# Kernel tuning notes

Hardware: AMD Instinct MI355X
Metric: run time of the kernel (lower is better)

## Reference

```python
import jax, jax.numpy as jnp
import numpy as np

SEQ_LEN = 4096
EMBED_DIM = 1024
NUM_HEADS = 16  # head_dim = 64


def setup_inputs() -> dict:
    key = jax.random.key(0)
    k0, k1, k2 = jax.random.split(key, 3)
    std = 0.02
    x = jax.random.normal(k0, (SEQ_LEN, EMBED_DIM), dtype=jnp.float32)
    # torch Linear convention: weight [out_features, in_features], y = x @ W.T + b
    W_qkv = jax.random.normal(k1, (3 * EMBED_DIM, EMBED_DIM), dtype=jnp.float32) * std
    b_qkv = jnp.zeros((3 * EMBED_DIM,), dtype=jnp.float32)
    W_out = jax.random.normal(k2, (EMBED_DIM, EMBED_DIM), dtype=jnp.float32) * std
    b_out = jnp.zeros((EMBED_DIM,), dtype=jnp.float32)
    return {"input": x, "W_qkv": W_qkv, "b_qkv": b_qkv, "W_out": W_out, "b_out": b_out}


def reference(input, W_qkv, b_qkv, W_out, b_out):
    S, E = input.shape
    H = NUM_HEADS
    Dh = E // H
    # fused QKV projection: [S, 3E]
    projected = input @ W_qkv.T + b_qkv
    q, k, v = jnp.split(projected, 3, axis=1)          # each [S, E]
    q = q.reshape(S, H, Dh)
    k = k.reshape(S, H, Dh)
    v = v.reshape(S, H, Dh)
    # unscaled attention (the original applies no 1/sqrt(d) scaling)
    scores = jnp.einsum('shd,thd->hst', q, k)          # [H, S, S] -- full matrix in HBM
    probs = jax.nn.softmax(scores, axis=-1)
    out = jnp.einsum('hst,thd->shd', probs, v)         # [S, H, Dh]
    out = out.reshape(S, E)
    return out @ W_out.T + b_out
```

## Files before the change

kernel.cpp:

```cpp
#include <hip/hip_runtime.h>

typedef unsigned short u16;
typedef short    bf16x8 __attribute__((ext_vector_type(8)));
typedef u16      u16x8  __attribute__((ext_vector_type(8)));
typedef u16      u16x4  __attribute__((ext_vector_type(4)));
typedef float    f32x4  __attribute__((ext_vector_type(4)));
typedef unsigned u32x2  __attribute__((ext_vector_type(2)));

__device__ __forceinline__ u16 f2bf(float f) {
  unsigned x = __float_as_uint(f);
  unsigned r = x + 0x7fffu + ((x >> 16) & 1u);
  return (u16)(r >> 16);
}
__device__ __forceinline__ float bf2f(u16 u) {
  return __uint_as_float(((unsigned)u) << 16);
}
__device__ __forceinline__ float exp2v(float x) {
  float r;
  asm("v_exp_f32 %0, %1" : "=v"(r) : "v"(x));
  return r;
}

__global__ __launch_bounds__(256) void cast3(const float* __restrict__ x,
                                             const float* __restrict__ wq,
                                             const float* __restrict__ wo,
                                             u16* __restrict__ xb,
                                             u16* __restrict__ wqb,
                                             u16* __restrict__ wob) {
  int b = blockIdx.x;
  const float* s; u16* d; int i;
  if (b < 4096)      { s = x;  d = xb;  i = b * 256 + threadIdx.x; }
  else if (b < 7168) { s = wq; d = wqb; i = (b - 4096) * 256 + threadIdx.x; }
  else               { s = wo; d = wob; i = (b - 7168) * 256 + threadIdx.x; }
  f32x4 v = ((const f32x4*)s)[i];
  u16x4 o;
  o[0] = f2bf(v[0]); o[1] = f2bf(v[1]); o[2] = f2bf(v[2]); o[3] = f2bf(v[3]);
  ((u16x4*)d)[i] = o;
}

template<int N, int K, bool OUTF32, bool SCALEQ, bool VSPLIT>
__global__ __launch_bounds__(256) void gemm_bt(const u16* __restrict__ A,
                                               const u16* __restrict__ B,
                                               const float* __restrict__ bias,
                                               void* __restrict__ Cout,
                                               u16* __restrict__ vtout) {
  __shared__ __align__(16) u16 smem[16384];
  const int tid = threadIdx.x;
  const int flat = blockIdx.y * gridDim.x + blockIdx.x;
  const int q8 = (gridDim.x * gridDim.y) >> 3;
  const int sw = (flat & 7) * q8 + (flat >> 3);
  const int m0 = (sw / gridDim.x) * 128, n0 = (sw % gridDim.x) * 128;
  const int wave = tid >> 6, lane = tid & 63;
  const int c = lane & 15, g = lane >> 4;
  const int wm = (wave >> 1) * 64, wn = (wave & 1) * 64;
  f32x4 acc[4][4] = {};

  const int sr = wave * 16 + (lane >> 2);
  const int sc = (lane & 3) * 8;

  auto stage = [&](int buf, int k0) {
#pragma unroll
    for (int j = 0; j < 2; j++) {
      __builtin_amdgcn_global_load_lds(
        (const __attribute__((address_space(1))) void*)(A + (size_t)(m0 + j * 64 + sr) * K + k0 + sc),
        (__attribute__((address_space(3))) void*)&smem[buf * 4096 + (j * 64 + wave * 16) * 32], 16, 0, 0);
      __builtin_amdgcn_global_load_lds(
        (const __attribute__((address_space(1))) void*)(B + (size_t)(n0 + j * 64 + sr) * K + k0 + sc),
        (__attribute__((address_space(3))) void*)&smem[8192 + buf * 4096 + (j * 64 + wave * 16) * 32], 16, 0, 0);
    }
  };

  stage(0, 0);
  __syncthreads();

  const int nT = K / 32;
  for (int t = 0; t < nT; ++t) {
    const int buf = t & 1;
    if (t + 1 < nT) stage(buf ^ 1, (t + 1) * 32);
    bf16x8 af[4], bfr[4];
#pragma unroll
    for (int m = 0; m < 4; m++)
      af[m]  = *(const bf16x8*)&smem[buf * 4096 + (wm + m * 16 + c) * 32 + g * 8];
#pragma unroll
    for (int n = 0; n < 4; n++)
      bfr[n] = *(const bf16x8*)&smem[8192 + buf * 4096 + (wn + n * 16 + c) * 32 + g * 8];
#pragma unroll
    for (int m = 0; m < 4; m++)
#pragma unroll
      for (int n = 0; n < 4; n++)
        acc[m][n] = __builtin_amdgcn_mfma_f32_16x16x32_bf16(af[m], bfr[n], acc[m][n], 0, 0, 0);
    __syncthreads();
  }

  if (VSPLIT && n0 >= 2048) {
#pragma unroll
    for (int n = 0; n < 4; n++) {
      float bv = bias[n0 + wn + n * 16 + c];
#pragma unroll
      for (int m = 0; m < 4; m++) {
#pragma unroll
        for (int r = 0; r < 4; r++) {
          int nl = wn + n * 16 + c;
          int ml = wm + m * 16 + g * 4 + r;
          int Gs = (ml >> 3) ^ (nl & 15);
          smem[nl * 128 + (Gs << 3) + (ml & 7)] = f2bf(acc[m][n][r] + bv);
        }
      }
    }
    __syncthreads();
    const int nl = tid >> 1, half = tid & 1;
    const int hd = n0 - 2048 + nl;
    u16* dst = vtout + (size_t)hd * 4096 + m0 + half * 64;
#pragma unroll
    for (int Gj = 0; Gj < 8; Gj++) {
      int G = half * 8 + Gj;
      u16x8 v = *(const u16x8*)&smem[nl * 128 + ((G ^ (nl & 15)) << 3)];
      *(u16x8*)(dst + Gj * 8) = v;
    }
    return;
  }

  const float qscale = (SCALEQ && n0 < 1024) ? 1.44269504f : 1.0f;
#pragma unroll
  for (int n = 0; n < 4; n++) {
    float bv = bias[n0 + wn + n * 16 + c];
#pragma unroll
    for (int m = 0; m < 4; m++) {
#pragma unroll
      for (int r = 0; r < 4; r++) {
        float val = (acc[m][n][r] + bv) * qscale;
        int row = m0 + wm + m * 16 + g * 4 + r;
        int col = n0 + wn + n * 16 + c;
        if constexpr (OUTF32) ((float*)Cout)[(size_t)row * N + col] = val;
        else                  ((u16*)Cout)[(size_t)row * N + col] = f2bf(val);
      }
    }
  }
}

__global__ __launch_bounds__(256, 4) void attn_kernel(const u16* __restrict__ qkv,
                                                      const u16* __restrict__ vt,
                                                      u16* __restrict__ pb0,
                                                      u16* __restrict__ pb1,
                                                      float* __restrict__ lb0,
                                                      float* __restrict__ lb1) {
  const int bid = blockIdx.x;
  const int kk  = bid & 1;
  const int qt  = (bid >> 1) & 31;
  const int h   = bid >> 6;
  const int q0  = qt * 128;
  const int kbase = kk * 2048;
  const int tid = threadIdx.x;
  const int wave = tid >> 6, lane = tid & 63;
  const int c = lane & 15, g = lane >> 4;
  const int qw = q0 + wave * 32;

  __shared__ __align__(16) u16 kls[2][64 * 64];
  __shared__ __align__(16) u16 vls[2][64 * 64];
  __shared__ __align__(16) unsigned plds[4][16 * 32];
  unsigned* pw = plds[wave];
  const int pswz = (c & 7) << 2;

  const u16* Kg = qkv + 1024 + h * 64;
  const u16* Vg = vt + (size_t)h * 64 * 4096;

  const int srow = lane >> 3, sgr = lane & 7;
  const int gc = sgr ^ (srow & 7);
  const u16* kp = Kg + (size_t)(kbase + wave * 16 + srow) * 3072 + gc * 8;
  const u16* vp = Vg + (size_t)(wave * 16 + srow) * 4096 + kbase + gc * 8;

  auto stage = [&](int buf, const u16* kpp, const u16* vpp) {
#pragma unroll
    for (int j = 0; j < 2; j++) {
      __builtin_amdgcn_global_load_lds(
        (const __attribute__((address_space(1))) void*)(kpp + (size_t)j * 8 * 3072),
        (__attribute__((address_space(3))) void*)&kls[buf][(wave * 16 + j * 8) * 64], 16, 0, 0);
      __builtin_amdgcn_global_load_lds(
        (const __attribute__((address_space(1))) void*)(vpp + (size_t)j * 8 * 4096),
        (__attribute__((address_space(3))) void*)&vls[buf][(wave * 16 + j * 8) * 64], 16, 0, 0);
    }
  };

  bf16x8 qf[2][2];
#pragma unroll
  for (int qs = 0; qs < 2; qs++)
#pragma unroll
    for (int dc = 0; dc < 2; dc++)
      qf[qs][dc] = *(const bf16x8*)&qkv[(size_t)(qw + qs * 16 + c) * 3072 + h * 64 + dc * 32 + g * 8];

  bf16x8 ones;
#pragma unroll
  for (int j = 0; j < 8; j++) ones[j] = (short)0x3F80;

  f32x4 o0[4] = {}, o1[4] = {};
  f32x4 accl0 = {}, accl1 = {};
  const f32x4 minit = {-16.f, -16.f, -16.f, -16.f};

  auto softmax = [&](f32x4 (&st)[4]) {
#pragma unroll
    for (int ks = 0; ks < 4; ks++) {
      float p0 = exp2v(st[ks][0]), p1 = exp2v(st[ks][1]);
      float p2 = exp2v(st[ks][2]), p3 = exp2v(st[ks][3]);
      unsigned w0, w1;
      asm("v_cvt_pk_bf16_f32 %0, %1, %2" : "=v"(w0) : "v"(p0), "v"(p1));
      asm("v_cvt_pk_bf16_f32 %0, %1, %2" : "=v"(w1) : "v"(p2), "v"(p3));
      u32x2 w2 = {w0, w1};
      *(u32x2*)&pw[c * 32 + ((ks * 8 + g * 2) ^ pswz)] = w2;
    }
  };

  stage(0, kp, vp);
  kp += (size_t)64 * 3072; vp += 64;
  __syncthreads();

  for (int t = 0; t < 32; ++t) {
    const int buf = t & 1;
    if (t + 1 < 32) {
      stage(buf ^ 1, kp, vp);
      kp += (size_t)64 * 3072; vp += 64;
    }

    f32x4 st0[4], st1[4];
    __builtin_amdgcn_s_setprio(1);
#pragma unroll
    for (int ks = 0; ks < 4; ks++) {
      bf16x8 kf0 = *(const bf16x8*)&kls[buf][(ks * 16 + c) * 64 + ((g ^ (c & 7)) << 3)];
      bf16x8 kf1 = *(const bf16x8*)&kls[buf][(ks * 16 + c) * 64 + (((4 + g) ^ (c & 7)) << 3)];
      f32x4 s0 = __builtin_amdgcn_mfma_f32_16x16x32_bf16(kf0, qf[0][0], minit, 0, 0, 0);
      st0[ks]  = __builtin_amdgcn_mfma_f32_16x16x32_bf16(kf1, qf[0][1], s0, 0, 0, 0);
      f32x4 s1 = __builtin_amdgcn_mfma_f32_16x16x32_bf16(kf0, qf[1][0], minit, 0, 0, 0);
      st1[ks]  = __builtin_amdgcn_mfma_f32_16x16x32_bf16(kf1, qf[1][1], s1, 0, 0, 0);
    }
    __builtin_amdgcn_s_setprio(0);

    softmax(st0);
    bf16x8 pa0[2], pa1[2];
#pragma unroll
    for (int hh = 0; hh < 2; hh++)
      pa0[hh] = *(const bf16x8*)&pw[c * 32 + ((hh * 16 + g * 4) ^ pswz)];
    softmax(st1);
#pragma unroll
    for (int hh = 0; hh < 2; hh++)
      pa1[hh] = *(const bf16x8*)&pw[c * 32 + ((hh * 16 + g * 4) ^ pswz)];

    __builtin_amdgcn_s_setprio(1);
#pragma unroll
    for (int k2 = 0; k2 < 2; k2++) {
      accl0 = __builtin_amdgcn_mfma_f32_16x16x32_bf16(pa0[k2], ones, accl0, 0, 0, 0);
      accl1 = __builtin_amdgcn_mfma_f32_16x16x32_bf16(pa1[k2], ones, accl1, 0, 0, 0);
#pragma unroll
      for (int dt = 0; dt < 4; dt++) {
        bf16x8 vf = *(const bf16x8*)&vls[buf][(dt * 16 + c) * 64 + (((k2 * 4 + g) ^ (c & 7)) << 3)];
        o0[dt] = __builtin_amdgcn_mfma_f32_16x16x32_bf16(pa0[k2], vf, o0[dt], 0, 0, 0);
        o1[dt] = __builtin_amdgcn_mfma_f32_16x16x32_bf16(pa1[k2], vf, o1[dt], 0, 0, 0);
      }
    }
    __builtin_amdgcn_s_setprio(0);
    __syncthreads();
  }

  u16* pb = kk ? pb1 : pb0;
  float* lb = (kk ? lb1 : lb0) + h * 4096 + qw;
  u16* pq = pb + (size_t)qw * 1024 + h * 64;

#pragma unroll
  for (int r = 0; r < 4; r++) {
    int rl = g * 4 + r;
    float inv0 = 1.0f / accl0[r];
    float inv1 = 1.0f / accl1[r];
#pragma unroll
    for (int dt = 0; dt < 4; dt++) {
      pq[(size_t)rl * 1024 + dt * 16 + c]        = f2bf(o0[dt][r] * inv0);
      pq[(size_t)(16 + rl) * 1024 + dt * 16 + c] = f2bf(o1[dt][r] * inv1);
    }
    if (c == 0) {
      lb[rl]      = accl0[r];
      lb[16 + rl] = accl1[r];
    }
  }
}

__global__ __launch_bounds__(256) void combine_kernel(u16* __restrict__ pb0,
                                                      const u16* __restrict__ pb1,
                                                      const float* __restrict__ lb0,
                                                      const float* __restrict__ lb1) {
  int t = blockIdx.x * 256 + threadIdx.x;
  int q = t >> 7;
  int c8 = t & 127;
  int h = c8 >> 3;
  float A = lb0[h * 4096 + q];
  float B = lb1[h * 4096 + q];
  float inv = 1.0f / (A + B);
  float w0 = A * inv, w1 = B * inv;
  size_t off = (size_t)q * 1024 + c8 * 8;
  u16x8 x0 = *(const u16x8*)(pb0 + off);
  u16x8 x1 = *(const u16x8*)(pb1 + off);
  u16x8 o;
#pragma unroll
  for (int e = 0; e < 8; e++)
    o[e] = f2bf(bf2f(x0[e]) * w0 + bf2f(x1[e]) * w1);
  *(u16x8*)(pb0 + off) = o;
}

extern "C" void kernel_launch(void* const* d_in, const int* in_sizes, int n_in,
                              void* d_out, int out_size, void* d_ws, size_t ws_size,
                              hipStream_t stream) {
  const float* x    = (const float*)d_in[0];
  const float* Wqkv = (const float*)d_in[1];
  const float* bqkv = (const float*)d_in[2];
  const float* Wout = (const float*)d_in[3];
  const float* bout = (const float*)d_in[4];

  char* ws = (char*)d_ws;
  u16* xb    = (u16*)(ws);
  u16* wqkvb = (u16*)(ws + (size_t)8  * (1u << 20));
  u16* woutb = (u16*)(ws + (size_t)14 * (1u << 20));
  u16* qkvb  = (u16*)(ws + (size_t)16 * (1u << 20));
  u16* vtb   = (u16*)(ws + (size_t)40 * (1u << 20));
  u16* pb0   = (u16*)(ws + (size_t)48 * (1u << 20));
  char* dob = (char*)d_out;
  u16*   pb1 = (u16*)dob;
  float* lb0 = (float*)(dob + (size_t)8 * (1u << 20));
  float* lb1 = lb0 + 65536;

  cast3<<<8192, 256, 0, stream>>>(x, Wqkv, Wout, xb, wqkvb, woutb);

  gemm_bt<3072, 1024, false, true, true><<<dim3(24, 32), 256, 0, stream>>>(
      xb, wqkvb, bqkv, qkvb, vtb);

  attn_kernel<<<1024, 256, 0, stream>>>(qkvb, vtb, pb0, pb1, lb0, lb1);

  combine_kernel<<<2048, 256, 0, stream>>>(pb0, pb1, lb0, lb1);

  gemm_bt<1024, 1024, true, false, false><<<dim3(8, 32), 256, 0, stream>>>(
      pb0, woutb, bout, d_out, nullptr);
}
```

Baseline: 170.7 us.

## Load K fragments directly from global into registers, bypassing LDS staging

K tiles are no longer staged through shared memory with global_load_lds. Each wave now loads its K MFMA fragments straight from global memory into registers, prefetching the next tile right after the QK MFMAs. This removes the LDS traffic and LDS footprint for K, which may allow higher occupancy. In exchange, all four waves redundantly fetch the same K data from global/L2, and the uncoalesced 16-byte row-strided loads add register pressure.

```diff
diff --git a/kernel.cpp b/kernel.cpp
--- a/kernel.cpp
+++ b/kernel.cpp
@@ -155,26 +155,20 @@
   const int c = lane & 15, g = lane >> 4;
   const int qw = q0 + wave * 32;
 
-  __shared__ __align__(16) u16 kls[2][64 * 64];
   __shared__ __align__(16) u16 vls[2][64 * 64];
   __shared__ __align__(16) unsigned plds[4][16 * 32];
   unsigned* pw = plds[wave];
   const int pswz = (c & 7) << 2;
 
-  const u16* Kg = qkv + 1024 + h * 64;
   const u16* Vg = vt + (size_t)h * 64 * 4096;
 
   const int srow = lane >> 3, sgr = lane & 7;
   const int gc = sgr ^ (srow & 7);
-  const u16* kp = Kg + (size_t)(kbase + wave * 16 + srow) * 3072 + gc * 8;
   const u16* vp = Vg + (size_t)(wave * 16 + srow) * 4096 + kbase + gc * 8;
 
-  auto stage = [&](int buf, const u16* kpp, const u16* vpp) {
+  auto stage = [&](int buf, const u16* vpp) {
 #pragma unroll
     for (int j = 0; j < 2; j++) {
-      __builtin_amdgcn_global_load_lds(
-        (const __attribute__((address_space(1))) void*)(kpp + (size_t)j * 8 * 3072),
-        (__attribute__((address_space(3))) void*)&kls[buf][(wave * 16 + j * 8) * 64], 16, 0, 0);
       __builtin_amdgcn_global_load_lds(
         (const __attribute__((address_space(1))) void*)(vpp + (size_t)j * 8 * 4096),
         (__attribute__((address_space(3))) void*)&vls[buf][(wave * 16 + j * 8) * 64], 16, 0, 0);
@@ -209,29 +203,45 @@
     }
   };
 
-  stage(0, kp, vp);
-  kp += (size_t)64 * 3072; vp += 64;
+  const u16* kdir = qkv + 1024 + h * 64 + (size_t)(kbase + c) * 3072 + g * 8;
+  bf16x8 k0[4], k1[4];
+#pragma unroll
+  for (int ks = 0; ks < 4; ks++) {
+    k0[ks] = *(const bf16x8*)(kdir + (size_t)(ks * 16) * 3072);
+    k1[ks] = *(const bf16x8*)(kdir + (size_t)(ks * 16) * 3072 + 32);
+  }
+  kdir += (size_t)64 * 3072;
+
+  stage(0, vp);
+  vp += 64;
   __syncthreads();
 
   for (int t = 0; t < 32; ++t) {
     const int buf = t & 1;
     if (t + 1 < 32) {
-      stage(buf ^ 1, kp, vp);
-      kp += (size_t)64 * 3072; vp += 64;
+      stage(buf ^ 1, vp);
+      vp += 64;
     }
 
     f32x4 st0[4], st1[4];
     __builtin_amdgcn_s_setprio(1);
 #pragma unroll
     for (int ks = 0; ks < 4; ks++) {
-      bf16x8 kf0 = *(const bf16x8*)&kls[buf][(ks * 16 + c) * 64 + ((g ^ (c & 7)) << 3)];
-      bf16x8 kf1 = *(const bf16x8*)&kls[buf][(ks * 16 + c) * 64 + (((4 + g) ^ (c & 7)) << 3)];
-      f32x4 s0 = __builtin_amdgcn_mfma_f32_16x16x32_bf16(kf0, qf[0][0], minit, 0, 0, 0);
-      st0[ks]  = __builtin_amdgcn_mfma_f32_16x16x32_bf16(kf1, qf[0][1], s0, 0, 0, 0);
-      f32x4 s1 = __builtin_amdgcn_mfma_f32_16x16x32_bf16(kf0, qf[1][0], minit, 0, 0, 0);
-      st1[ks]  = __builtin_amdgcn_mfma_f32_16x16x32_bf16(kf1, qf[1][1], s1, 0, 0, 0);
+      f32x4 s0 = __builtin_amdgcn_mfma_f32_16x16x32_bf16(k0[ks], qf[0][0], minit, 0, 0, 0);
+      st0[ks]  = __builtin_amdgcn_mfma_f32_16x16x32_bf16(k1[ks], qf[0][1], s0, 0, 0, 0);
+      f32x4 s1 = __builtin_amdgcn_mfma_f32_16x16x32_bf16(k0[ks], qf[1][0], minit, 0, 0, 0);
+      st1[ks]  = __builtin_amdgcn_mfma_f32_16x16x32_bf16(k1[ks], qf[1][1], s1, 0, 0, 0);
     }
     __builtin_amdgcn_s_setprio(0);
+
+    if (t + 1 < 32) {
+#pragma unroll
+      for (int ks = 0; ks < 4; ks++) {
+        k0[ks] = *(const bf16x8*)(kdir + (size_t)(ks * 16) * 3072);
+        k1[ks] = *(const bf16x8*)(kdir + (size_t)(ks * 16) * 3072 + 32);
+      }
+      kdir += (size_t)64 * 3072;
+    }
 
     softmax(st0);
     bf16x8 pa0[2], pa1[2];
```

New measurement: 265.2 us. 1.55x slower.
